# Kernel optimization log

Hardware: AMD Instinct MI355X
Metric: run time of the kernel (lower is better)

The kernel has to match this reference:

```python
import jax, jax.numpy as jnp
import numpy as np
import math


def setup_inputs() -> dict:
    key = jax.random.key(0)
    k1, k2 = jax.random.split(key)
    q = jax.random.normal(k1, (2, 8, 2048, 64), dtype=jnp.float32)
    v = jax.random.normal(k2, (2, 8, 2048, 64), dtype=jnp.float32)
    return {"q": q, "v": v}


def reference(q, v):
    # q, v: [B, H, L, D]. Softmax-free Gaussian-kernel attention.
    # squared L2 distance via expanded form: ||qi||^2 + ||qj||^2 - 2 qi.qj
    # (same math as the original's broadcasted difference, without the
    #  O(B,H,L,L,D) intermediate)
    d = q.shape[-1]
    sq = jnp.sum(q * q, axis=-1)                      # [B, H, L]
    dots = jnp.einsum('bhid,bhjd->bhij', q, q)        # [B, H, L, L]
    sq_l2 = sq[..., :, None] + sq[..., None, :] - 2.0 * dots
    score = jnp.exp(-1.0 / (2.0 * math.sqrt(d)) * sq_l2)  # [B, H, L, L]
    return jnp.einsum('bhij,bhjd->bhid', score, v)    # [B, H, L, D]
```

## Files before the change

### kernel.cpp

```cpp
#include <hip/hip_runtime.h>
#include <hip/hip_bf16.h>
#include <stdint.h>

typedef __bf16 bf16_t;
typedef bf16_t bf16x8 __attribute__((ext_vector_type(8)));
typedef float f32x16 __attribute__((ext_vector_type(16)));
typedef float fvec4 __attribute__((ext_vector_type(4)));
typedef unsigned int u32x4v __attribute__((ext_vector_type(4)));

#define LEN 2048
#define DIM 64
#define NH  16

#define C_L8  0.18033688011112043f
#define C_L16 0.09016844005556021f

__device__ __forceinline__ float fexp2(float x) {
#if __has_builtin(__builtin_amdgcn_exp2f)
  return __builtin_amdgcn_exp2f(x);
#else
  return exp2f(x);
#endif
}

__device__ __forceinline__ unsigned pk2(float lo, float hi) {
  union { bf16_t h; unsigned short u; } a, b;
  a.h = (bf16_t)lo; b.h = (bf16_t)hi;
  return (unsigned)a.u | ((unsigned)b.u << 16);
}

__device__ __forceinline__ void glds16(const void* g, void* l) {
  __builtin_amdgcn_global_load_lds(
      (const __attribute__((address_space(1))) void*)g,
      (__attribute__((address_space(3))) void*)l, 16, 0, 0);
}

__device__ __forceinline__ int swk(int row, int b) {
  return row * 128 + (b ^ ((row & 7) << 4));
}
__device__ __forceinline__ int swv(int row, int b) {
  return row * 256 + (b ^ ((row & 7) << 4));
}

__global__ __launch_bounds__(256) void prepass(
    const float* __restrict__ q, const float* __restrict__ v,
    bf16_t* __restrict__ kb, bf16_t* __restrict__ vt, float* __restrict__ sqw) {
  __shared__ float wlds[64];
  const int b = blockIdx.x;
  const int h = b >> 5, jb = b & 31;
  const int t = threadIdx.x;
  const float* qh = q + ((size_t)h * LEN + jb * 64) * DIM;
  const float* vh = v + ((size_t)h * LEN + jb * 64) * DIM;

  {
    const int j = t >> 2, d0 = (t & 3) * 16;
    const float* qp = qh + j * DIM + d0;
    float s = 0.f;
    bf16x8 o0, o1;
#pragma unroll
    for (int e = 0; e < 8; ++e) {
      bf16_t hh = (bf16_t)qp[e]; o0[e] = hh; float f = (float)hh; s += f * f;
    }
#pragma unroll
    for (int e = 0; e < 8; ++e) {
      bf16_t hh = (bf16_t)qp[8 + e]; o1[e] = hh; float f = (float)hh; s += f * f;
    }
    bf16_t* kp = kb + ((size_t)h * LEN + jb * 64 + j) * DIM + d0;
    *(bf16x8*)kp = o0;
    *(bf16x8*)(kp + 8) = o1;
    s += __shfl_xor(s, 1);
    s += __shfl_xor(s, 2);
    if ((t & 3) == 0) {
      wlds[j] = fexp2(-s * C_L16);
      sqw[h * LEN + jb * 64 + j] = s * C_L16;
    }
  }
  __syncthreads();
  {
    const int d = t & 63, jg = t >> 6;
    float vv[16];
#pragma unroll
    for (int e = 0; e < 16; ++e) vv[e] = vh[(jg * 16 + e) * DIM + d];
    bf16x8 o0, o1;
#pragma unroll
    for (int e = 0; e < 8; ++e)  o0[e] = (bf16_t)(vv[e] * wlds[jg * 16 + e]);
#pragma unroll
    for (int e = 0; e < 8; ++e)  o1[e] = (bf16_t)(vv[8 + e] * wlds[jg * 16 + 8 + e]);
    bf16_t* vp = vt + ((size_t)h * DIM + d) * LEN + jb * 64 + jg * 16;
    *(bf16x8*)vp = o0;
    *(bf16x8*)(vp + 8) = o1;
  }
}

__global__ __launch_bounds__(512, 4) void soft_attn_main(
    const bf16_t* __restrict__ kb, const bf16_t* __restrict__ vt,
    const float* __restrict__ sqw, float* __restrict__ out) {
  __shared__ __align__(16) char smem[65536];

  const int tid  = threadIdx.x;
  const int lane = tid & 63;
  const int wave = tid >> 6;
  const int rg   = wave & 1;
  const int par  = wave >> 1;
  const int g    = lane >> 5;
  const int nn   = lane & 31;

  const int b  = blockIdx.x;
  const int wg = ((b & 7) << 6) | (b >> 3);
  const int bh = wg >> 5;
  const int qb = wg & 31;

  const bf16_t* kh  = kb + (size_t)bh * LEN * DIM;
  const bf16_t* vth = vt + (size_t)bh * DIM * LEN;

  const int qrow = qb * 64 + rg * 32 + nn;
  bf16x8 qf[4];
  {
    const bf16_t* qp = kh + (size_t)qrow * DIM;
#pragma unroll
    for (int kc = 0; kc < 4; ++kc)
      qf[kc] = *(const bf16x8*)(qp + kc * 16 + g * 8);
  }
  const float hq = sqw[bh * LEN + qrow];

  const bf16_t* ksrc[2];
  const bf16_t* vsrc[2];
#pragma unroll
  for (int s = 0; s < 2; ++s) {
    const int krow = wave * 16 + s * 8 + (lane >> 3);
    const int kby  = ((lane & 7) * 16) ^ ((lane >> 3) << 4);
    ksrc[s] = kh + (size_t)krow * DIM + (kby >> 1);
    const int vrow = wave * 8 + s * 4 + (lane >> 4);
    const int vby  = ((lane & 15) * 16) ^ ((vrow & 7) << 4);
    vsrc[s] = vth + (size_t)vrow * LEN + (vby >> 1);
  }
  char* kdst = smem + wave * 2048;
  char* vdst = smem + 32768 + wave * 2048;

  f32x16 acc0 = {};
  f32x16 acc1 = {};

#pragma unroll
  for (int s = 0; s < 2; ++s) {
    glds16(ksrc[s], kdst + s * 1024);
    glds16(vsrc[s], vdst + s * 1024);
  }
#pragma unroll
  for (int s = 0; s < 2; ++s) {
    glds16(ksrc[s] + (size_t)128 * DIM, kdst + 16384 + s * 1024);
    glds16(vsrc[s] + (size_t)128,       vdst + 16384 + s * 1024);
  }

  for (int it = 0; it < 16; ++it) {
    if (it < 15) {
      asm volatile("s_waitcnt vmcnt(4)" ::: "memory");
    } else {
      asm volatile("s_waitcnt vmcnt(0)" ::: "memory");
    }
    __builtin_amdgcn_sched_barrier(0);
    __builtin_amdgcn_s_barrier();
    __builtin_amdgcn_sched_barrier(0);

    const int buf = it & 1;
    const char* kb0 = smem + buf * 16384;
    const char* vb0 = smem + 32768 + buf * 16384;

    f32x16 t = {};
    __builtin_amdgcn_s_setprio(1);
#pragma unroll
    for (int kc = 0; kc < 4; ++kc) {
      bf16x8 kf = *(const bf16x8*)(kb0 + swk(par * 32 + nn, kc * 32 + g * 16));
      t = __builtin_amdgcn_mfma_f32_32x32x16_bf16(kf, qf[kc], t, 0, 0, 0);
    }
    __builtin_amdgcn_s_setprio(0);

    unsigned P[8];
#pragma unroll
    for (int e = 0; e < 8; ++e) {
      float s0 = fexp2(__builtin_fmaf(t[2 * e],     C_L8, -hq));
      float s1 = fexp2(__builtin_fmaf(t[2 * e + 1], C_L8, -hq));
      P[e] = pk2(s0, s1);
    }
    asm volatile("v_permlane32_swap_b32 %0, %1" : "+v"(P[0]), "+v"(P[2]));
    asm volatile("v_permlane32_swap_b32 %0, %1" : "+v"(P[1]), "+v"(P[3]));
    asm volatile("v_permlane32_swap_b32 %0, %1" : "+v"(P[4]), "+v"(P[6]));
    asm volatile("v_permlane32_swap_b32 %0, %1" : "+v"(P[5]), "+v"(P[7]));
    u32x4v f0v = { P[0], P[1], P[2], P[3] };
    u32x4v f1v = { P[4], P[5], P[6], P[7] };
    bf16x8 af0 = __builtin_bit_cast(bf16x8, f0v);
    bf16x8 af1 = __builtin_bit_cast(bf16x8, f1v);

    {
      bf16x8 v0 = *(const bf16x8*)(vb0 + swv(nn,      par * 64 + g * 16));
      bf16x8 v1 = *(const bf16x8*)(vb0 + swv(32 + nn, par * 64 + g * 16));
      bf16x8 v2 = *(const bf16x8*)(vb0 + swv(nn,      par * 64 + 32 + g * 16));
      bf16x8 v3 = *(const bf16x8*)(vb0 + swv(32 + nn, par * 64 + 32 + g * 16));
      __builtin_amdgcn_s_setprio(1);
      acc0 = __builtin_amdgcn_mfma_f32_32x32x16_bf16(af0, v0, acc0, 0, 0, 0);
      acc1 = __builtin_amdgcn_mfma_f32_32x32x16_bf16(af0, v1, acc1, 0, 0, 0);
      acc0 = __builtin_amdgcn_mfma_f32_32x32x16_bf16(af1, v2, acc0, 0, 0, 0);
      acc1 = __builtin_amdgcn_mfma_f32_32x32x16_bf16(af1, v3, acc1, 0, 0, 0);
      __builtin_amdgcn_s_setprio(0);
    }

    __builtin_amdgcn_sched_barrier(0);
    __builtin_amdgcn_s_barrier();
    __builtin_amdgcn_sched_barrier(0);

    if (it + 2 < 16) {
#pragma unroll
      for (int s = 0; s < 2; ++s) {
        glds16(ksrc[s] + (size_t)(it + 2) * 128 * DIM, kdst + buf * 16384 + s * 1024);
        glds16(vsrc[s] + (size_t)(it + 2) * 128,       vdst + buf * 16384 + s * 1024);
      }
    }
  }

  float* xb = (float*)smem;
  if (par != 0) {
    float* dst = xb + ((par - 1) * 2 + rg) * 2048;
#pragma unroll
    for (int r = 0; r < 16; ++r) {
      dst[r * 64 + lane]        = acc0[r];
      dst[(16 + r) * 64 + lane] = acc1[r];
    }
  }
  __syncthreads();
  if (par == 0) {
    float* op = out + ((size_t)bh * LEN + qb * 64 + rg * 32) * DIM;
#pragma unroll
    for (int r = 0; r < 16; ++r) {
      const int row = (r & 3) + 8 * (r >> 2) + 4 * g;
      float a0 = acc0[r], a1 = acc1[r];
#pragma unroll
      for (int p = 1; p < 4; ++p) {
        const float* sb = xb + ((p - 1) * 2 + rg) * 2048;
        a0 += sb[r * 64 + lane];
        a1 += sb[(16 + r) * 64 + lane];
      }
      op[(size_t)row * DIM + nn]      = a0;
      op[(size_t)row * DIM + 32 + nn] = a1;
    }
  }
}

__device__ __forceinline__ int swfb(int row, int byte) {
  return row * 128 + (byte ^ ((row & 7) << 4));
}

__global__ __launch_bounds__(512, 2) void soft_attn_fb(
    const float* __restrict__ q, const float* __restrict__ v,
    float* __restrict__ out) {
  __shared__ __align__(16) char smem[33280];
  const int tid = threadIdx.x;
  const int lane = tid & 63;
  const int wave = tid >> 6;
  const int rg = wave & 3;
  const int parity = wave >> 2;
  const int tp = tid & 255;
  const int g = lane >> 5;
  const int nn = lane & 31;
  const int wg = ((blockIdx.x & 7) << 5) | (blockIdx.x >> 3);
  const int bh = wg >> 4;
  const int qb = wg & 15;
  const float* qh = q + (size_t)bh * LEN * DIM;
  const float* vh = v + (size_t)bh * LEN * DIM;
  char* kbufp = smem + parity * 8192;
  char* vbufp = smem + 16384 + parity * 8192;
  float* wkp = (float*)(smem + 32768) + parity * 64;
  const int qrow = qb * 128 + rg * 32 + nn;
  bf16x8 qf[4];
  float sq = 0.f;
  {
    const float* qp = qh + (size_t)qrow * DIM;
#pragma unroll
    for (int kc = 0; kc < 4; ++kc) {
      const int d0 = kc * 16 + g * 8;
      fvec4 x = *(const fvec4*)(qp + d0);
      fvec4 y = *(const fvec4*)(qp + d0 + 4);
      bf16x8 t;
#pragma unroll
      for (int e = 0; e < 4; ++e) {
        bf16_t h0 = (bf16_t)x[e]; t[e] = h0; float f0 = (float)h0; sq += f0 * f0;
        bf16_t h1 = (bf16_t)y[e]; t[e + 4] = h1; float f1 = (float)h1; sq += f1 * f1;
      }
      qf[kc] = t;
    }
  }
  sq += __shfl_xor(sq, 32);
  const float hq = sq * C_L16;
  f32x16 acc0 = {};
  f32x16 acc1 = {};
  for (int it = 0; it < 16; ++it) {
    const int jt = it * 2 + parity;
    const float* kg = qh + (size_t)jt * 64 * DIM;
    const float* vg = vh + (size_t)jt * 64 * DIM;
    __syncthreads();
#pragma unroll
    for (int s = 0; s < 2; ++s) {
      const int c = tp + 256 * s;
      const int j = c >> 3;
      const int d0 = (c & 7) * 8;
      fvec4 x = *(const fvec4*)(kg + j * DIM + d0);
      fvec4 y = *(const fvec4*)(kg + j * DIM + d0 + 4);
      bf16x8 t; float p = 0.f;
#pragma unroll
      for (int e = 0; e < 4; ++e) {
        bf16_t h0 = (bf16_t)x[e]; t[e] = h0; float f0 = (float)h0; p += f0 * f0;
        bf16_t h1 = (bf16_t)y[e]; t[e + 4] = h1; float f1 = (float)h1; p += f1 * f1;
      }
      *(bf16x8*)(kbufp + swfb(j, d0 * 2)) = t;
      p += __shfl_xor(p, 1);
      p += __shfl_xor(p, 2);
      p += __shfl_xor(p, 4);
      if ((lane & 7) == 0) wkp[j] = fexp2(-p * C_L16);
    }
    __syncthreads();
    float vl[2][8];
    const int vd = tp & 63;
    const int vw = tp >> 6;
#pragma unroll
    for (int s = 0; s < 2; ++s) {
      const int j0 = vw * 8 + 32 * s;
      const float* vp = vg + j0 * DIM + vd;
#pragma unroll
      for (int r = 0; r < 8; ++r) vl[s][r] = vp[r * DIM];
    }
    bf16x8 af[4];
#pragma unroll
    for (int jsub = 0; jsub < 2; ++jsub) {
      f32x16 t = {};
#pragma unroll
      for (int kc = 0; kc < 4; ++kc) {
        bf16x8 kf = *(const bf16x8*)(kbufp + swfb(jsub * 32 + nn, kc * 32 + g * 16));
        t = __builtin_amdgcn_mfma_f32_32x32x16_bf16(kf, qf[kc], t, 0, 0, 0);
      }
      unsigned P[8];
#pragma unroll
      for (int e = 0; e < 8; ++e) {
        float s0 = fexp2(__builtin_fmaf(t[2 * e], C_L8, -hq));
        float s1 = fexp2(__builtin_fmaf(t[2 * e + 1], C_L8, -hq));
        P[e] = pk2(s0, s1);
      }
      asm volatile("v_permlane32_swap_b32 %0, %1" : "+v"(P[0]), "+v"(P[2]));
      asm volatile("v_permlane32_swap_b32 %0, %1" : "+v"(P[1]), "+v"(P[3]));
      asm volatile("v_permlane32_swap_b32 %0, %1" : "+v"(P[4]), "+v"(P[6]));
      asm volatile("v_permlane32_swap_b32 %0, %1" : "+v"(P[5]), "+v"(P[7]));
      u32x4v f0v = { P[0], P[1], P[2], P[3] };
      u32x4v f1v = { P[4], P[5], P[6], P[7] };
      af[jsub * 2] = __builtin_bit_cast(bf16x8, f0v);
      af[jsub * 2 + 1] = __builtin_bit_cast(bf16x8, f1v);
    }
#pragma unroll
    for (int s = 0; s < 2; ++s) {
      const int j0 = vw * 8 + 32 * s;
      bf16x8 t;
#pragma unroll
      for (int r = 0; r < 8; ++r) {
        float w = wkp[j0 + r];
        t[r] = (bf16_t)(vl[s][r] * w);
      }
      *(bf16x8*)(vbufp + swfb(vd, j0 * 2)) = t;
    }
    __syncthreads();
#pragma unroll
    for (int kc = 0; kc < 4; ++kc) {
      bf16x8 v0 = *(const bf16x8*)(vbufp + swfb(nn, kc * 32 + g * 16));
      bf16x8 v1 = *(const bf16x8*)(vbufp + swfb(32 + nn, kc * 32 + g * 16));
      acc0 = __builtin_amdgcn_mfma_f32_32x32x16_bf16(af[kc], v0, acc0, 0, 0, 0);
      acc1 = __builtin_amdgcn_mfma_f32_32x32x16_bf16(af[kc], v1, acc1, 0, 0, 0);
    }
  }
  __syncthreads();
  float* xb = (float*)smem + rg * 2048;
  if (parity == 1) {
#pragma unroll
    for (int r = 0; r < 16; ++r) {
      xb[r * 64 + lane] = acc0[r];
      xb[(16 + r) * 64 + lane] = acc1[r];
    }
  }
  __syncthreads();
  if (parity == 0) {
    float* op = out + ((size_t)bh * LEN + qb * 128 + rg * 32) * DIM;
#pragma unroll
    for (int r = 0; r < 16; ++r) {
      const int row = (r & 3) + 8 * (r >> 2) + 4 * g;
      op[(size_t)row * DIM + nn] = acc0[r] + xb[r * 64 + lane];
      op[(size_t)row * DIM + 32 + nn] = acc1[r] + xb[(16 + r) * 64 + lane];
    }
  }
}

extern "C" void kernel_launch(void* const* d_in, const int* in_sizes, int n_in,
                              void* d_out, int out_size, void* d_ws, size_t ws_size,
                              hipStream_t stream) {
  const float* q = (const float*)d_in[0];
  const float* v = (const float*)d_in[1];
  float* out = (float*)d_out;
  (void)in_sizes; (void)n_in; (void)out_size;

  const size_t KB_BYTES = (size_t)NH * LEN * DIM * 2;
  const size_t NEED = KB_BYTES * 2 + (size_t)NH * LEN * 4;
  if (ws_size >= NEED) {
    bf16_t* kb  = (bf16_t*)d_ws;
    bf16_t* vt  = (bf16_t*)((char*)d_ws + KB_BYTES);
    float*  sqw = (float*)((char*)d_ws + KB_BYTES * 2);
    prepass<<<dim3(512), dim3(256), 0, stream>>>(q, v, kb, vt, sqw);
    soft_attn_main<<<dim3(512), dim3(512), 0, stream>>>(kb, vt, sqw, out);
  } else {
    soft_attn_fb<<<dim3(256), dim3(512), 0, stream>>>(q, v, out);
  }
}
```

Measured before the change: 95.56 us.

## Double query rows per block and switch to triple-buffered K/V with one barrier

```diff
diff --git a/kernel.cpp b/kernel.cpp
--- a/kernel.cpp
+++ b/kernel.cpp
@@ -92,10 +92,10 @@
   }
 }
 
-__global__ __launch_bounds__(512, 4) void soft_attn_main(
+__global__ __launch_bounds__(512, 2) void soft_attn_main(
     const bf16_t* __restrict__ kb, const bf16_t* __restrict__ vt,
     const float* __restrict__ sqw, float* __restrict__ out) {
-  __shared__ __align__(16) char smem[65536];
+  __shared__ __align__(16) char smem[98304];
 
   const int tid  = threadIdx.x;
   const int lane = tid & 63;
@@ -106,22 +106,26 @@
   const int nn   = lane & 31;
 
   const int b  = blockIdx.x;
-  const int wg = ((b & 7) << 6) | (b >> 3);
-  const int bh = wg >> 5;
-  const int qb = wg & 31;
+  const int wg = ((b & 7) << 5) | (b >> 3);
+  const int bh = wg >> 4;
+  const int qb = wg & 15;
 
   const bf16_t* kh  = kb + (size_t)bh * LEN * DIM;
   const bf16_t* vth = vt + (size_t)bh * DIM * LEN;
 
-  const int qrow = qb * 64 + rg * 32 + nn;
-  bf16x8 qf[4];
+  const int qrow0 = qb * 128 + rg * 64 + nn;
+  bf16x8 qf0[4], qf1[4];
   {
-    const bf16_t* qp = kh + (size_t)qrow * DIM;
-#pragma unroll
-    for (int kc = 0; kc < 4; ++kc)
-      qf[kc] = *(const bf16x8*)(qp + kc * 16 + g * 8);
-  }
-  const float hq = sqw[bh * LEN + qrow];
+    const bf16_t* qp0 = kh + (size_t)qrow0 * DIM;
+    const bf16_t* qp1 = kh + (size_t)(qrow0 + 32) * DIM;
+#pragma unroll
+    for (int kc = 0; kc < 4; ++kc) {
+      qf0[kc] = *(const bf16x8*)(qp0 + kc * 16 + g * 8);
+      qf1[kc] = *(const bf16x8*)(qp1 + kc * 16 + g * 8);
+    }
+  }
+  const float hq0 = sqw[bh * LEN + qrow0];
+  const float hq1 = sqw[bh * LEN + qrow0 + 32];
 
   const bf16_t* ksrc[2];
   const bf16_t* vsrc[2];
@@ -135,10 +139,9 @@
     vsrc[s] = vth + (size_t)vrow * LEN + (vby >> 1);
   }
   char* kdst = smem + wave * 2048;
-  char* vdst = smem + 32768 + wave * 2048;
-
-  f32x16 acc0 = {};
-  f32x16 acc1 = {};
+  char* vdst = smem + 49152 + wave * 2048;
+
+  f32x16 acc00 = {}, acc01 = {}, acc10 = {}, acc11 = {};
 
 #pragma unroll
   for (int s = 0; s < 2; ++s) {
@@ -151,6 +154,7 @@
     glds16(vsrc[s] + (size_t)128,       vdst + 16384 + s * 1024);
   }
 
+  int bufo = 0;
   for (int it = 0; it < 16; ++it) {
     if (it < 15) {
       asm volatile("s_waitcnt vmcnt(4)" ::: "memory");
@@ -161,34 +165,60 @@
     __builtin_amdgcn_s_barrier();
     __builtin_amdgcn_sched_barrier(0);
 
-    const int buf = it & 1;
-    const char* kb0 = smem + buf * 16384;
-    const char* vb0 = smem + 32768 + buf * 16384;
-
-    f32x16 t = {};
+    const char* kb0 = smem + bufo;
+    const char* vb0 = smem + 49152 + bufo;
+
+    bf16x8 kf0 = *(const bf16x8*)(kb0 + swk(par * 32 + nn, 0 * 32 + g * 16));
+    bf16x8 kf1 = *(const bf16x8*)(kb0 + swk(par * 32 + nn, 1 * 32 + g * 16));
+    bf16x8 kf2 = *(const bf16x8*)(kb0 + swk(par * 32 + nn, 2 * 32 + g * 16));
+    bf16x8 kf3 = *(const bf16x8*)(kb0 + swk(par * 32 + nn, 3 * 32 + g * 16));
+    f32x16 t0 = {}, t1 = {};
     __builtin_amdgcn_s_setprio(1);
-#pragma unroll
-    for (int kc = 0; kc < 4; ++kc) {
-      bf16x8 kf = *(const bf16x8*)(kb0 + swk(par * 32 + nn, kc * 32 + g * 16));
-      t = __builtin_amdgcn_mfma_f32_32x32x16_bf16(kf, qf[kc], t, 0, 0, 0);
-    }
+    t0 = __builtin_amdgcn_mfma_f32_32x32x16_bf16(kf0, qf0[0], t0, 0, 0, 0);
+    t1 = __builtin_amdgcn_mfma_f32_32x32x16_bf16(kf0, qf1[0], t1, 0, 0, 0);
+    t0 = __builtin_amdgcn_mfma_f32_32x32x16_bf16(kf1, qf0[1], t0, 0, 0, 0);
+    t1 = __builtin_amdgcn_mfma_f32_32x32x16_bf16(kf1, qf1[1], t1, 0, 0, 0);
+    t0 = __builtin_amdgcn_mfma_f32_32x32x16_bf16(kf2, qf0[2], t0, 0, 0, 0);
+    t1 = __builtin_amdgcn_mfma_f32_32x32x16_bf16(kf2, qf1[2], t1, 0, 0, 0);
+    t0 = __builtin_amdgcn_mfma_f32_32x32x16_bf16(kf3, qf0[3], t0, 0, 0, 0);
+    t1 = __builtin_amdgcn_mfma_f32_32x32x16_bf16(kf3, qf1[3], t1, 0, 0, 0);
     __builtin_amdgcn_s_setprio(0);
 
-    unsigned P[8];
-#pragma unroll
-    for (int e = 0; e < 8; ++e) {
-      float s0 = fexp2(__builtin_fmaf(t[2 * e],     C_L8, -hq));
-      float s1 = fexp2(__builtin_fmaf(t[2 * e + 1], C_L8, -hq));
-      P[e] = pk2(s0, s1);
-    }
-    asm volatile("v_permlane32_swap_b32 %0, %1" : "+v"(P[0]), "+v"(P[2]));
-    asm volatile("v_permlane32_swap_b32 %0, %1" : "+v"(P[1]), "+v"(P[3]));
-    asm volatile("v_permlane32_swap_b32 %0, %1" : "+v"(P[4]), "+v"(P[6]));
-    asm volatile("v_permlane32_swap_b32 %0, %1" : "+v"(P[5]), "+v"(P[7]));
-    u32x4v f0v = { P[0], P[1], P[2], P[3] };
-    u32x4v f1v = { P[4], P[5], P[6], P[7] };
-    bf16x8 af0 = __builtin_bit_cast(bf16x8, f0v);
-    bf16x8 af1 = __builtin_bit_cast(bf16x8, f1v);
+    bf16x8 af00, af01, af10, af11;
+    {
+      unsigned P[8];
+#pragma unroll
+      for (int e = 0; e < 8; ++e) {
+        float s0 = fexp2(__builtin_fmaf(t0[2 * e],     C_L8, -hq0));
+        float s1 = fexp2(__builtin_fmaf(t0[2 * e + 1], C_L8, -hq0));
+        P[e] = pk2(s0, s1);
+      }
+      asm volatile("v_permlane32_swap_b32 %0, %1" : "+v"(P[0]), "+v"(P[2]));
+      asm volatile("v_permlane32_swap_b32 %0, %1" : "+v"(P[1]), "+v"(P[3]));
+      asm volatile("v_permlane32_swap_b32 %0, %1" : "+v"(P[4]), "+v"(P[6]));
+      asm volatile("v_permlane32_swap_b32 %0, %1" : "+v"(P[5]), "+v"(P[7]));
+      u32x4v f0v = { P[0], P[1], P[2], P[3] };
+      u32x4v f1v = { P[4], P[5], P[6], P[7] };
+      af00 = __builtin_bit_cast(bf16x8, f0v);
+      af01 = __builtin_bit_cast(bf16x8, f1v);
+    }
+    {
+      unsigned P[8];
+#pragma unroll
+      for (int e = 0; e < 8; ++e) {
+        float s0 = fexp2(__builtin_fmaf(t1[2 * e],     C_L8, -hq1));
+        float s1 = fexp2(__builtin_fmaf(t1[2 * e + 1], C_L8, -hq1));
+        P[e] = pk2(s0, s1);
+      }
+      asm volatile("v_permlane32_swap_b32 %0, %1" : "+v"(P[0]), "+v"(P[2]));
+      asm volatile("v_permlane32_swap_b32 %0, %1" : "+v"(P[1]), "+v"(P[3]));
+      asm volatile("v_permlane32_swap_b32 %0, %1" : "+v"(P[4]), "+v"(P[6]));
+      asm volatile("v_permlane32_swap_b32 %0, %1" : "+v"(P[5]), "+v"(P[7]));
+      u32x4v f0v = { P[0], P[1], P[2], P[3] };
+      u32x4v f1v = { P[4], P[5], P[6], P[7] };
+      af10 = __builtin_bit_cast(bf16x8, f0v);
+      af11 = __builtin_bit_cast(bf16x8, f1v);
+    }
 
     {
       bf16x8 v0 = *(const bf16x8*)(vb0 + swv(nn,      par * 64 + g * 16));
@@ -196,50 +226,64 @@
       bf16x8 v2 = *(const bf16x8*)(vb0 + swv(nn,      par * 64 + 32 + g * 16));
       bf16x8 v3 = *(const bf16x8*)(vb0 + swv(32 + nn, par * 64 + 32 + g * 16));
       __builtin_amdgcn_s_setprio(1);
-      acc0 = __builtin_amdgcn_mfma_f32_32x32x16_bf16(af0, v0, acc0, 0, 0, 0);
-      acc1 = __builtin_amdgcn_mfma_f32_32x32x16_bf16(af0, v1, acc1, 0, 0, 0);
-      acc0 = __builtin_amdgcn_mfma_f32_32x32x16_bf16(af1, v2, acc0, 0, 0, 0);
-      acc1 = __builtin_amdgcn_mfma_f32_32x32x16_bf16(af1, v3, acc1, 0, 0, 0);
+      acc00 = __builtin_amdgcn_mfma_f32_32x32x16_bf16(af00, v0, acc00, 0, 0, 0);
+      acc01 = __builtin_amdgcn_mfma_f32_32x32x16_bf16(af00, v1, acc01, 0, 0, 0);
+      acc10 = __builtin_amdgcn_mfma_f32_32x32x16_bf16(af10, v0, acc10, 0, 0, 0);
+      acc11 = __builtin_amdgcn_mfma_f32_32x32x16_bf16(af10, v1, acc11, 0, 0, 0);
+      acc00 = __builtin_amdgcn_mfma_f32_32x32x16_bf16(af01, v2, acc00, 0, 0, 0);
+      acc01 = __builtin_amdgcn_mfma_f32_32x32x16_bf16(af01, v3, acc01, 0, 0, 0);
+      acc10 = __builtin_amdgcn_mfma_f32_32x32x16_bf16(af11, v2, acc10, 0, 0, 0);
+      acc11 = __builtin_amdgcn_mfma_f32_32x32x16_bf16(af11, v3, acc11, 0, 0, 0);
       __builtin_amdgcn_s_setprio(0);
     }
 
-    __builtin_amdgcn_sched_barrier(0);
-    __builtin_amdgcn_s_barrier();
-    __builtin_amdgcn_sched_barrier(0);
-
     if (it + 2 < 16) {
+      int nbo = bufo + 32768; if (nbo >= 49152) nbo -= 49152;
 #pragma unroll
       for (int s = 0; s < 2; ++s) {
-        glds16(ksrc[s] + (size_t)(it + 2) * 128 * DIM, kdst + buf * 16384 + s * 1024);
-        glds16(vsrc[s] + (size_t)(it + 2) * 128,       vdst + buf * 16384 + s * 1024);
-      }
-    }
-  }
-
+        glds16(ksrc[s] + (size_t)(it + 2) * 128 * DIM, kdst + nbo + s * 1024);
+        glds16(vsrc[s] + (size_t)(it + 2) * 128,       vdst + nbo + s * 1024);
+      }
+    }
+
+    bufo += 16384; if (bufo >= 49152) bufo = 0;
+  }
+
+  __syncthreads();
   float* xb = (float*)smem;
   if (par != 0) {
-    float* dst = xb + ((par - 1) * 2 + rg) * 2048;
+    const int slot = (par - 1) * 4 + rg * 2;
+    float* d0 = xb + slot * 2048;
+    float* d1 = xb + (slot + 1) * 2048;
 #pragma unroll
     for (int r = 0; r < 16; ++r) {
-      dst[r * 64 + lane]        = acc0[r];
-      dst[(16 + r) * 64 + lane] = acc1[r];
+      d0[r * 64 + lane]        = acc00[r];
+      d0[1024 + r * 64 + lane] = acc01[r];
+      d1[r * 64 + lane]        = acc10[r];
+      d1[1024 + r * 64 + lane] = acc11[r];
     }
   }
   __syncthreads();
   if (par == 0) {
-    float* op = out + ((size_t)bh * LEN + qb * 64 + rg * 32) * DIM;
+    float* op = out + ((size_t)bh * LEN + qb * 128 + rg * 64) * DIM;
 #pragma unroll
     for (int r = 0; r < 16; ++r) {
       const int row = (r & 3) + 8 * (r >> 2) + 4 * g;
-      float a0 = acc0[r], a1 = acc1[r];
+      float a00 = acc00[r], a01 = acc01[r], a10 = acc10[r], a11 = acc11[r];
 #pragma unroll
       for (int p = 1; p < 4; ++p) {
-        const float* sb = xb + ((p - 1) * 2 + rg) * 2048;
-        a0 += sb[r * 64 + lane];
-        a1 += sb[(16 + r) * 64 + lane];
-      }
-      op[(size_t)row * DIM + nn]      = a0;
-      op[(size_t)row * DIM + 32 + nn] = a1;
+        const int slot = (p - 1) * 4 + rg * 2;
+        const float* s0 = xb + slot * 2048;
+        const float* s1 = xb + (slot + 1) * 2048;
+        a00 += s0[r * 64 + lane];
+        a01 += s0[1024 + r * 64 + lane];
+        a10 += s1[r * 64 + lane];
+        a11 += s1[1024 + r * 64 + lane];
+      }
+      op[(size_t)row * DIM + nn]               = a00;
+      op[(size_t)row * DIM + 32 + nn]          = a01;
+      op[(size_t)(32 + row) * DIM + nn]        = a10;
+      op[(size_t)(32 + row) * DIM + 32 + nn]   = a11;
     }
   }
 }
@@ -407,7 +451,7 @@
     bf16_t* vt  = (bf16_t*)((char*)d_ws + KB_BYTES);
     float*  sqw = (float*)((char*)d_ws + KB_BYTES * 2);
     prepass<<<dim3(512), dim3(256), 0, stream>>>(q, v, kb, vt, sqw);
-    soft_attn_main<<<dim3(512), dim3(512), 0, stream>>>(kb, vt, sqw, out);
+    soft_attn_main<<<dim3(256), dim3(512), 0, stream>>>(kb, vt, sqw, out);
   } else {
     soft_attn_fb<<<dim3(256), dim3(512), 0, stream>>>(q, v, out);
   }
```

Result: no change. 95.29 us (-0.3%).
